# Optimization experiments

Measured on AMD Instinct MI355X. Metric: run time of the kernel, lower is better.

## Reference

```python
import jax, jax.numpy as jnp
import numpy as np

NEG_SLOPE = 0.2


def _gcn_conv(x, edge_index, W, b):
    # Standard GCNConv: y = D^-1/2 (A + I) D^-1/2 (x W) + b
    N = x.shape[0]
    loop = jnp.arange(N, dtype=edge_index.dtype)
    src = jnp.concatenate([edge_index[0], loop])  # [E+N]
    dst = jnp.concatenate([edge_index[1], loop])  # [E+N]
    deg = jax.ops.segment_sum(jnp.ones_like(dst, dtype=x.dtype), dst, num_segments=N)
    dinv = jnp.where(deg > 0, jax.lax.rsqrt(deg), 0.0)
    norm = dinv[src] * dinv[dst]                  # [E+N]
    h = x @ W                                     # [N, out] dense GEMM
    msg = h[src] * norm[:, None]                  # irregular gather, [E+N, out]
    agg = jax.ops.segment_sum(msg, dst, num_segments=N)  # irregular scatter
    return agg + b


def setup_inputs() -> dict:
    key = jax.random.key(0)
    ks = jax.random.split(key, 5)
    N, E, d_in, d_hid = 50000, 800000, 256, 512
    s = lambda fan_in, fan_out: np.sqrt(6.0 / (fan_in + fan_out))
    return {
        "x": jax.random.normal(ks[0], (N, d_in), dtype=jnp.float32),
        "edge_index": jax.random.randint(ks[1], (2, E), 0, N, dtype=jnp.int64),
        "W_gcn": jax.random.uniform(ks[2], (d_in, d_hid), jnp.float32, -s(d_in, d_hid), s(d_in, d_hid)),
        "b_gcn": jnp.zeros((d_hid,), jnp.float32),
        "W2": jax.random.uniform(ks[3], (d_hid, d_hid), jnp.float32, -s(d_hid, d_hid), s(d_hid, d_hid)),
        "b2": jnp.zeros((d_hid,), jnp.float32),
        "W_out": jax.random.uniform(ks[4], (d_hid, 1), jnp.float32, -s(d_hid, 1), s(d_hid, 1)),
        "b_out": jnp.zeros((1,), jnp.float32),
    }


def reference(x, edge_index, W_gcn, b_gcn, W2, b2, W_out, b_out):
    h = _gcn_conv(x, edge_index, W_gcn, b_gcn)           # [N, 512]
    h = jax.nn.leaky_relu(h, NEG_SLOPE)
    h = jax.nn.leaky_relu(h @ W2 + b2, NEG_SLOPE)        # [N, 512]
    return h @ W_out + b_out                             # [N, 1]
```

## Files before the change

kernel.cpp:

```cpp
#include <hip/hip_runtime.h>

#define D_IN  256
#define D_HID 512
#define NEG_SLOPE 0.2f
#define CAP 64
#define OVF_MAX 65536

typedef __attribute__((ext_vector_type(8))) short short8;
typedef __attribute__((ext_vector_type(4))) float floatx4;

__device__ __forceinline__ unsigned short f2bf(float f) {
    unsigned int u = __float_as_uint(f);
    u += 0x7fffu + ((u >> 16) & 1u);
    return (unsigned short)(u >> 16);
}
__device__ __forceinline__ float bf2f(unsigned short u) {
    return __uint_as_float(((unsigned int)u) << 16);
}

__device__ __forceinline__ int eidx(const void* ei, long pos, int is64) {
    return is64 ? (int)((const long long*)ei)[pos] : ((const int*)ei)[pos];
}

__global__ __launch_bounds__(256) void k_init(const float* __restrict__ x,
                                              unsigned short* __restrict__ xb,
                                              int* __restrict__ deg, int N,
                                              const unsigned int* __restrict__ ei,
                                              int npairs, int* flag, int* ovfcnt,
                                              const float* __restrict__ b_out,
                                              float* __restrict__ out,
                                              const float* __restrict__ Wa,
                                              unsigned short* __restrict__ Wat,
                                              const float* __restrict__ Wb,
                                              unsigned short* __restrict__ Wbt,
                                              long xthreads) {
    __shared__ float tl[64][65];
    int b = blockIdx.x;
    if (b < 96) {
        const float* W; unsigned short* Wt; int K, Nc, tk, tn;
        if (b < 32) { W = Wa; Wt = Wat; K = 256; Nc = 512; tk = b & 3; tn = b >> 2; }
        else { b -= 32; W = Wb; Wt = Wbt; K = 512; Nc = 512; tk = b & 7; tn = b >> 3; }
        int k0 = tk * 64, n0 = tn * 64;
        int c = threadIdx.x & 63;
        int r0 = threadIdx.x >> 6;
#pragma unroll
        for (int i = 0; i < 16; ++i) {
            int r = r0 + i * 4;
            tl[r][c] = W[(long)(k0 + r) * Nc + n0 + c];
        }
        __syncthreads();
#pragma unroll
        for (int i = 0; i < 16; ++i) {
            int r = r0 + i * 4;
            Wt[(long)(n0 + r) * K + k0 + c] = f2bf(tl[c][r]);
        }
        return;
    }
    if (b == 96) {
        __shared__ int nz;
        if (threadIdx.x == 0) nz = 0;
        __syncthreads();
        for (int p = threadIdx.x; p < npairs; p += blockDim.x)
            if (ei[2 * p + 1] != 0) nz = 1;
        __syncthreads();
        if (threadIdx.x == 0) { *flag = nz ? 0 : 1; *ovfcnt = 0; }
    }
    long t = (long)(b - 96) * 256 + threadIdx.x;
    if (t < xthreads) {
        long i = t * 4;
        float4 v = *(const float4*)(x + i);
        ushort4 o;
        o.x = f2bf(v.x); o.y = f2bf(v.y); o.z = f2bf(v.z); o.w = f2bf(v.w);
        *(ushort4*)(xb + i) = o;
    }
    if (t < N) { deg[t] = 0; out[t] = b_out[0]; }
}

__global__ void k_degfill(const void* __restrict__ ei, const int* __restrict__ flag,
                          int* __restrict__ deg, int* __restrict__ esrc,
                          int2* __restrict__ ovf, int* __restrict__ ovfcnt, int E) {
    int e = blockIdx.x * blockDim.x + threadIdx.x;
    if (e >= E) return;
    int is64 = *flag;
    int s = eidx(ei, e, is64), d = eidx(ei, (long)E + e, is64);
    int r = atomicAdd(&deg[d], 1);
    if (r < CAP) {
        esrc[d * CAP + r] = s;
    } else {
        int p = atomicAdd(ovfcnt, 1);
        if (p < OVF_MAX) ovf[p] = make_int2(d, s);
    }
}

__global__ __launch_bounds__(256) void k_dinv(const int* __restrict__ deg,
                                              float* __restrict__ dinv, int N) {
    int i = blockIdx.x * blockDim.x + threadIdx.x;
    if (i < N) dinv[i] = rsqrtf(1.0f + (float)deg[i]);
}

__global__ __launch_bounds__(256) void k_gather(const unsigned short* __restrict__ xb,
                                                const int* __restrict__ deg,
                                                const int* __restrict__ esrc,
                                                const float* __restrict__ dinv,
                                                const int2* __restrict__ ovf,
                                                const int* __restrict__ ovfcnt,
                                                unsigned short* __restrict__ aggb, int N) {
    int node = blockIdx.x * 4 + (threadIdx.x >> 6);
    int lane = threadIdx.x & 63;
    if (node >= N) return;
    int half = lane >> 5;
    int li   = lane & 31;
    int colofs = li * 8;
    float di = dinv[node];

    float a[8];
    {
        short8 v = *(const short8*)(xb + (long)node * D_IN + colofs);
#pragma unroll
        for (int j = 0; j < 8; ++j)
            a[j] = (half == 0) ? di * bf2f((unsigned short)v[j]) : 0.f;
    }

    int cnt = deg[node];
    if (cnt > CAP) cnt = CAP;
    int beg = node * CAP, end = beg + cnt;
    int e = beg;
    for (; e + 8 <= end; e += 8) {
        int s0 = esrc[e + half];
        int s1 = esrc[e + 2 + half];
        int s2 = esrc[e + 4 + half];
        int s3 = esrc[e + 6 + half];
        float w0 = dinv[s0], w1 = dinv[s1], w2 = dinv[s2], w3 = dinv[s3];
        short8 u0 = *(const short8*)(xb + (long)s0 * D_IN + colofs);
        short8 u1 = *(const short8*)(xb + (long)s1 * D_IN + colofs);
        short8 u2 = *(const short8*)(xb + (long)s2 * D_IN + colofs);
        short8 u3 = *(const short8*)(xb + (long)s3 * D_IN + colofs);
#pragma unroll
        for (int j = 0; j < 8; ++j)
            a[j] += w0 * bf2f((unsigned short)u0[j]) + w1 * bf2f((unsigned short)u1[j])
                  + w2 * bf2f((unsigned short)u2[j]) + w3 * bf2f((unsigned short)u3[j]);
    }
    for (; e < end; e += 2) {
        int j0 = e + half;
        int jj = (j0 < end) ? j0 : end - 1;
        int s = esrc[jj];
        float w = (j0 < end) ? dinv[s] : 0.f;
        short8 u = *(const short8*)(xb + (long)s * D_IN + colofs);
#pragma unroll
        for (int j = 0; j < 8; ++j)
            a[j] += w * bf2f((unsigned short)u[j]);
    }

    int oc = *ovfcnt;
    if (oc > OVF_MAX) oc = OVF_MAX;
    for (int i = 0; i < oc; ++i) {
        int2 p = ovf[i];
        if (p.x == node && half == 0) {
            float w = dinv[p.y];
            short8 u = *(const short8*)(xb + (long)p.y * D_IN + colofs);
#pragma unroll
            for (int j = 0; j < 8; ++j)
                a[j] += w * bf2f((unsigned short)u[j]);
        }
    }

#pragma unroll
    for (int j = 0; j < 8; ++j) a[j] += __shfl_xor(a[j], 32, 64);

    if (half == 0) {
        short8 o;
#pragma unroll
        for (int j = 0; j < 8; ++j) o[j] = (short)f2bf(a[j] * di);
        *(short8*)(aggb + (long)node * D_IN + colofs) = o;
    }
}

__device__ __forceinline__ void async_cp16(const unsigned short* gp, unsigned short* lp) {
    __builtin_amdgcn_global_load_lds((const __attribute__((address_space(1))) void*)gp,
                                     (__attribute__((address_space(3))) void*)lp, 16, 0, 0);
}

__device__ __forceinline__ void stage_sw64(const unsigned short* src, int strideK,
                                           int rowMax, unsigned short* lds, int tid) {
#pragma unroll
    for (int rr = 0; rr < 4; ++rr) {
        int c = rr * 256 + tid;
        int row = c >> 3;
        int ci = (c & 7) ^ (row & 7);
        if (row > rowMax) row = rowMax;
        async_cp16(src + (long)row * strideK + ci * 8, lds + c * 8);
    }
}

__device__ __forceinline__ bool map_block(int b, int M, int& m0, int& n0) {
    int x = b & 7, slot = b >> 3;
    int mt = x + 8 * (slot >> 2);
    m0 = mt * 128; n0 = (slot & 3) * 128;
    return m0 < M;
}

__device__ __forceinline__ void mfma_step(const unsigned short* As_,
                                          const unsigned short* Bs_,
                                          floatx4 acc[4][4],
                                          int wm, int wn, int r, int q, int xv) {
#pragma unroll
    for (int s = 0; s < 2; ++s) {
        int slotbase = s * 4 + q;
        short8 af[4], bf[4];
#pragma unroll
        for (int i = 0; i < 4; ++i)
            af[i] = *(const short8*)(As_ + (wm + i * 16 + r) * 64 + (slotbase ^ xv) * 8);
#pragma unroll
        for (int j = 0; j < 4; ++j)
            bf[j] = *(const short8*)(Bs_ + (wn + j * 16 + r) * 64 + (slotbase ^ xv) * 8);
#pragma unroll
        for (int i = 0; i < 4; ++i)
#pragma unroll
            for (int j = 0; j < 4; ++j)
                acc[i][j] = __builtin_amdgcn_mfma_f32_16x16x32_bf16(af[i], bf[j], acc[i][j], 0, 0, 0);
    }
}

#define GEMM_KLOOP(Ab, Bb, K, rmA)                                              \
    const int nt = (K) >> 6;                                                    \
    stage_sw64((Ab), (K), (rmA), As[0], tid);                                   \
    stage_sw64((Bb), (K), 127, Bs[0], tid);                                     \
    if (nt > 1) {                                                               \
        stage_sw64((Ab) + 64, (K), (rmA), As[1], tid);                          \
        stage_sw64((Bb) + 64, (K), 127, Bs[1], tid);                            \
    }                                                                           \
    for (int t = 0; t < nt; ++t) {                                              \
        const int cur = t & 1;                                                  \
        if (t + 1 < nt) asm volatile("s_waitcnt vmcnt(8)" ::: "memory");        \
        else            asm volatile("s_waitcnt vmcnt(0)" ::: "memory");        \
        __builtin_amdgcn_sched_barrier(0);                                      \
        __builtin_amdgcn_s_barrier();                                           \
        __builtin_amdgcn_sched_barrier(0);                                      \
        mfma_step(As[cur], Bs[cur], acc, wm, wn, r, q, xv);                     \
        __builtin_amdgcn_sched_barrier(0);                                      \
        __builtin_amdgcn_s_barrier();                                           \
        __builtin_amdgcn_sched_barrier(0);                                      \
        if (t + 2 < nt) {                                                       \
            stage_sw64((Ab) + (long)(t + 2) * 64, (K), (rmA), As[cur], tid);    \
            stage_sw64((Bb) + (long)(t + 2) * 64, (K), 127, Bs[cur], tid);      \
        }                                                                       \
    }

__global__ __launch_bounds__(256) void k_gemm_bf16(const unsigned short* __restrict__ A,
                                                   const unsigned short* __restrict__ Bt,
                                                   const float* __restrict__ bias,
                                                   unsigned short* __restrict__ C,
                                                   int M, int K) {
    __shared__ __align__(16) unsigned short As[2][128 * 64];
    __shared__ __align__(16) unsigned short Bs[2][128 * 64];
    __shared__ __align__(16) unsigned short Ep[32 * 128];
    const int tid  = threadIdx.x;
    const int lane = tid & 63, wave = tid >> 6;
    int m0, n0;
    if (!map_block(blockIdx.x, M, m0, n0)) return;
    const int r = lane & 15, q = lane >> 4;
    const int xv = r & 7;
    const int wm = (wave & 1) * 64, wn = (wave >> 1) * 64;
    const int band = wm >> 6;
    const int rmA = M - 1 - m0;
    const unsigned short* Ab = A + (long)m0 * K;
    const unsigned short* Bb = Bt + (long)n0 * K;

    floatx4 acc[4][4];
#pragma unroll
    for (int i = 0; i < 4; ++i)
#pragma unroll
        for (int j = 0; j < 4; ++j) acc[i][j] = (floatx4){0.f, 0.f, 0.f, 0.f};

    GEMM_KLOOP(Ab, Bb, K, rmA)

    float bv[4];
#pragma unroll
    for (int j = 0; j < 4; ++j) bv[j] = bias[n0 + wn + j * 16 + r];

#pragma unroll
    for (int i = 0; i < 4; ++i) {
#pragma unroll
        for (int j = 0; j < 4; ++j) {
#pragma unroll
            for (int t2 = 0; t2 < 4; ++t2) {
                float v = acc[i][j][t2] + bv[j];
                v = v > 0.f ? v : NEG_SLOPE * v;
                Ep[(band * 16 + q * 4 + t2) * 128 + wn + j * 16 + r] = f2bf(v);
            }
        }
        __syncthreads();
#pragma unroll
        for (int rr = 0; rr < 2; ++rr) {
            int c = rr * 256 + tid;
            int lrow = c >> 4, ccol = c & 15;
            int grow = m0 + (lrow >> 4) * 64 + i * 16 + (lrow & 15);
            if (grow < M) {
                short8 v = *(const short8*)(Ep + lrow * 128 + ccol * 8);
                *(short8*)(C + (long)grow * D_HID + n0 + ccol * 8) = v;
            }
        }
        __syncthreads();
    }
}

__global__ __launch_bounds__(256) void k_gemm2f(const unsigned short* __restrict__ A,
                                                const unsigned short* __restrict__ Bt,
                                                const float* __restrict__ bias,
                                                const float* __restrict__ wout,
                                                float* __restrict__ out,
                                                int M, int K) {
    __shared__ __align__(16) unsigned short As[2][128 * 64];
    __shared__ __align__(16) unsigned short Bs[2][128 * 64];
    const int tid  = threadIdx.x;
    const int lane = tid & 63, wave = tid >> 6;
    int m0, n0;
    if (!map_block(blockIdx.x, M, m0, n0)) return;
    const int r = lane & 15, q = lane >> 4;
    const int xv = r & 7;
    const int wm = (wave & 1) * 64, wn = (wave >> 1) * 64;
    const int rmA = M - 1 - m0;
    const unsigned short* Ab = A + (long)m0 * K;
    const unsigned short* Bb = Bt + (long)n0 * K;

    floatx4 acc[4][4];
#pragma unroll
    for (int i = 0; i < 4; ++i)
#pragma unroll
        for (int j = 0; j < 4; ++j) acc[i][j] = (floatx4){0.f, 0.f, 0.f, 0.f};

    GEMM_KLOOP(Ab, Bb, K, rmA)

    float bv[4], wv[4];
#pragma unroll
    for (int j = 0; j < 4; ++j) {
        int col = n0 + wn + j * 16 + r;
        bv[j] = bias[col];
        wv[j] = wout[col];
    }
#pragma unroll
    for (int i = 0; i < 4; ++i) {
#pragma unroll
        for (int t2 = 0; t2 < 4; ++t2) {
            float p = 0.f;
#pragma unroll
            for (int j = 0; j < 4; ++j) {
                float v = acc[i][j][t2] + bv[j];
                v = v > 0.f ? v : NEG_SLOPE * v;
                p += v * wv[j];
            }
            p += __shfl_xor(p, 8, 64);
            p += __shfl_xor(p, 4, 64);
            p += __shfl_xor(p, 2, 64);
            p += __shfl_xor(p, 1, 64);
            if (r == 0) {
                int row = m0 + wm + i * 16 + q * 4 + t2;
                if (row < M) atomicAdd(&out[row], p);
            }
        }
    }
}

extern "C" void kernel_launch(void* const* d_in, const int* in_sizes, int n_in,
                              void* d_out, int out_size, void* d_ws, size_t ws_size,
                              hipStream_t stream) {
    const float* x     = (const float*)d_in[0];
    const void*  ei    = d_in[1];
    const float* W_gcn = (const float*)d_in[2];
    const float* b_gcn = (const float*)d_in[3];
    const float* W2    = (const float*)d_in[4];
    const float* b2    = (const float*)d_in[5];
    const float* W_out = (const float*)d_in[6];
    const float* b_out = (const float*)d_in[7];
    float* out = (float*)d_out;

    const int N = in_sizes[0] / D_IN;
    const int E = in_sizes[1] / 2;

    char* w = (char*)d_ws;
    size_t off = 0;
    auto alloc = [&](size_t bytes) { char* p = w + off; off = (off + bytes + 255) & ~(size_t)255; return p; };
    int*            flag   = (int*)alloc(256);
    int*            ovfcnt = (int*)alloc(256);
    float*          dinv   = (float*)alloc((size_t)N * 4);
    int*            deg_i  = (int*)alloc((size_t)N * 4);
    int2*           ovf    = (int2*)alloc((size_t)OVF_MAX * 8);
    int*            esrc   = (int*)alloc((size_t)N * CAP * 4);
    unsigned short* xb     = (unsigned short*)alloc((size_t)N * D_IN * 2);
    unsigned short* aggb   = (unsigned short*)alloc((size_t)N * D_IN * 2);
    unsigned short* h1     = (unsigned short*)alloc((size_t)N * D_HID * 2);
    unsigned short* Wgt    = (unsigned short*)alloc((size_t)D_IN * D_HID * 2);
    unsigned short* W2t    = (unsigned short*)alloc((size_t)D_HID * D_HID * 2);

    int npairs = E < 2048 ? E : 2048;
    long xthreads = (long)N * D_IN / 4;
    int init_blocks = 96 + (int)((xthreads + 255) / 256);
    k_init<<<init_blocks, 256, 0, stream>>>(x, xb, deg_i, N, (const unsigned int*)ei,
                                            npairs, flag, ovfcnt, b_out, out,
                                            W_gcn, Wgt, W2, W2t, xthreads);

    k_degfill<<<(E + 255) / 256, 256, 0, stream>>>(ei, flag, deg_i, esrc, ovf, ovfcnt, E);
    k_dinv<<<(N + 255) / 256, 256, 0, stream>>>(deg_i, dinv, N);

    k_gather<<<(N + 3) / 4, 256, 0, stream>>>(xb, deg_i, esrc, dinv, ovf, ovfcnt, aggb, N);

    int mtiles = (N + 127) / 128;
    int gblocks = ((mtiles + 7) / 8) * 8 * 4;
    k_gemm_bf16<<<gblocks, 256, 0, stream>>>(aggb, Wgt, b_gcn, h1, N, D_IN);
    k_gemm2f<<<gblocks, 256, 0, stream>>>(h1, W2t, b2, W_out, out, N, D_HID);
}
```

Before: 281.2 us.

## Loop over all N-tiles per GEMM block and compute dinv inline

Each GEMM block now owns a full 128-row M-tile and loops over the four 128-column N-tiles itself, instead of one block per (M,N) tile. This lets the final GEMM reduce the output projection in shared memory and write out[] directly, dropping the atomics and the out initialization in k_init. The k_dinv kernel is removed; the gather recomputes rsqrt(1+deg) from deg on the fly. The launch grid shrinks by four times (about 391 blocks), which risks underfilling the GPU, and the A tile is re-streamed for every N-tile.

```diff
diff --git a/kernel.cpp b/kernel.cpp
--- a/kernel.cpp
+++ b/kernel.cpp
@@ -27,8 +27,6 @@
                                               int* __restrict__ deg, int N,
                                               const unsigned int* __restrict__ ei,
                                               int npairs, int* flag, int* ovfcnt,
-                                              const float* __restrict__ b_out,
-                                              float* __restrict__ out,
                                               const float* __restrict__ Wa,
                                               unsigned short* __restrict__ Wat,
                                               const float* __restrict__ Wb,
@@ -73,7 +71,7 @@
         o.x = f2bf(v.x); o.y = f2bf(v.y); o.z = f2bf(v.z); o.w = f2bf(v.w);
         *(ushort4*)(xb + i) = o;
     }
-    if (t < N) { deg[t] = 0; out[t] = b_out[0]; }
+    if (t < N) deg[t] = 0;
 }
 
 __global__ void k_degfill(const void* __restrict__ ei, const int* __restrict__ flag,
@@ -92,16 +90,9 @@
     }
 }
 
-__global__ __launch_bounds__(256) void k_dinv(const int* __restrict__ deg,
-                                              float* __restrict__ dinv, int N) {
-    int i = blockIdx.x * blockDim.x + threadIdx.x;
-    if (i < N) dinv[i] = rsqrtf(1.0f + (float)deg[i]);
-}
-
 __global__ __launch_bounds__(256) void k_gather(const unsigned short* __restrict__ xb,
                                                 const int* __restrict__ deg,
                                                 const int* __restrict__ esrc,
-                                                const float* __restrict__ dinv,
                                                 const int2* __restrict__ ovf,
                                                 const int* __restrict__ ovfcnt,
                                                 unsigned short* __restrict__ aggb, int N) {
@@ -111,7 +102,8 @@
     int half = lane >> 5;
     int li   = lane & 31;
     int colofs = li * 8;
-    float di = dinv[node];
+    int dn = deg[node];
+    float di = rsqrtf(1.0f + (float)dn);
 
     float a[8];
     {
@@ -121,8 +113,7 @@
             a[j] = (half == 0) ? di * bf2f((unsigned short)v[j]) : 0.f;
     }
 
-    int cnt = deg[node];
-    if (cnt > CAP) cnt = CAP;
+    int cnt = dn > CAP ? CAP : dn;
     int beg = node * CAP, end = beg + cnt;
     int e = beg;
     for (; e + 8 <= end; e += 8) {
@@ -130,7 +121,10 @@
         int s1 = esrc[e + 2 + half];
         int s2 = esrc[e + 4 + half];
         int s3 = esrc[e + 6 + half];
-        float w0 = dinv[s0], w1 = dinv[s1], w2 = dinv[s2], w3 = dinv[s3];
+        float w0 = rsqrtf(1.0f + (float)deg[s0]);
+        float w1 = rsqrtf(1.0f + (float)deg[s1]);
+        float w2 = rsqrtf(1.0f + (float)deg[s2]);
+        float w3 = rsqrtf(1.0f + (float)deg[s3]);
         short8 u0 = *(const short8*)(xb + (long)s0 * D_IN + colofs);
         short8 u1 = *(const short8*)(xb + (long)s1 * D_IN + colofs);
         short8 u2 = *(const short8*)(xb + (long)s2 * D_IN + colofs);
@@ -144,7 +138,7 @@
         int j0 = e + half;
         int jj = (j0 < end) ? j0 : end - 1;
         int s = esrc[jj];
-        float w = (j0 < end) ? dinv[s] : 0.f;
+        float w = (j0 < end) ? rsqrtf(1.0f + (float)deg[s]) : 0.f;
         short8 u = *(const short8*)(xb + (long)s * D_IN + colofs);
 #pragma unroll
         for (int j = 0; j < 8; ++j)
@@ -156,7 +150,7 @@
     for (int i = 0; i < oc; ++i) {
         int2 p = ovf[i];
         if (p.x == node && half == 0) {
-            float w = dinv[p.y];
+            float w = rsqrtf(1.0f + (float)deg[p.y]);
             short8 u = *(const short8*)(xb + (long)p.y * D_IN + colofs);
 #pragma unroll
             for (int j = 0; j < 8; ++j)
@@ -190,13 +184,6 @@
         if (row > rowMax) row = rowMax;
         async_cp16(src + (long)row * strideK + ci * 8, lds + c * 8);
     }
-}
-
-__device__ __forceinline__ bool map_block(int b, int M, int& m0, int& n0) {
-    int x = b & 7, slot = b >> 3;
-    int mt = x + 8 * (slot >> 2);
-    m0 = mt * 128; n0 = (slot & 3) * 128;
-    return m0 < M;
 }
 
 __device__ __forceinline__ void mfma_step(const unsigned short* As_,
@@ -256,51 +243,54 @@
     __shared__ __align__(16) unsigned short Ep[32 * 128];
     const int tid  = threadIdx.x;
     const int lane = tid & 63, wave = tid >> 6;
-    int m0, n0;
-    if (!map_block(blockIdx.x, M, m0, n0)) return;
+    const int m0 = blockIdx.x * 128;
+    if (m0 >= M) return;
     const int r = lane & 15, q = lane >> 4;
     const int xv = r & 7;
     const int wm = (wave & 1) * 64, wn = (wave >> 1) * 64;
     const int band = wm >> 6;
     const int rmA = M - 1 - m0;
     const unsigned short* Ab = A + (long)m0 * K;
-    const unsigned short* Bb = Bt + (long)n0 * K;
-
-    floatx4 acc[4][4];
-#pragma unroll
-    for (int i = 0; i < 4; ++i)
-#pragma unroll
-        for (int j = 0; j < 4; ++j) acc[i][j] = (floatx4){0.f, 0.f, 0.f, 0.f};
-
-    GEMM_KLOOP(Ab, Bb, K, rmA)
-
-    float bv[4];
-#pragma unroll
-    for (int j = 0; j < 4; ++j) bv[j] = bias[n0 + wn + j * 16 + r];
-
-#pragma unroll
-    for (int i = 0; i < 4; ++i) {
-#pragma unroll
-        for (int j = 0; j < 4; ++j) {
-#pragma unroll
-            for (int t2 = 0; t2 < 4; ++t2) {
-                float v = acc[i][j][t2] + bv[j];
-                v = v > 0.f ? v : NEG_SLOPE * v;
-                Ep[(band * 16 + q * 4 + t2) * 128 + wn + j * 16 + r] = f2bf(v);
+
+    for (int n0 = 0; n0 < D_HID; n0 += 128) {
+        const unsigned short* Bb = Bt + (long)n0 * K;
+
+        floatx4 acc[4][4];
+#pragma unroll
+        for (int i = 0; i < 4; ++i)
+#pragma unroll
+            for (int j = 0; j < 4; ++j) acc[i][j] = (floatx4){0.f, 0.f, 0.f, 0.f};
+
+        GEMM_KLOOP(Ab, Bb, K, rmA)
+
+        float bv[4];
+#pragma unroll
+        for (int j = 0; j < 4; ++j) bv[j] = bias[n0 + wn + j * 16 + r];
+
+#pragma unroll
+        for (int i = 0; i < 4; ++i) {
+#pragma unroll
+            for (int j = 0; j < 4; ++j) {
+#pragma unroll
+                for (int t2 = 0; t2 < 4; ++t2) {
+                    float v = acc[i][j][t2] + bv[j];
+                    v = v > 0.f ? v : NEG_SLOPE * v;
+                    Ep[(band * 16 + q * 4 + t2) * 128 + wn + j * 16 + r] = f2bf(v);
+                }
             }
-        }
-        __syncthreads();
-#pragma unroll
-        for (int rr = 0; rr < 2; ++rr) {
-            int c = rr * 256 + tid;
-            int lrow = c >> 4, ccol = c & 15;
-            int grow = m0 + (lrow >> 4) * 64 + i * 16 + (lrow & 15);
-            if (grow < M) {
-                short8 v = *(const short8*)(Ep + lrow * 128 + ccol * 8);
-                *(short8*)(C + (long)grow * D_HID + n0 + ccol * 8) = v;
+            __syncthreads();
+#pragma unroll
+            for (int rr = 0; rr < 2; ++rr) {
+                int c = rr * 256 + tid;
+                int lrow = c >> 4, ccol = c & 15;
+                int grow = m0 + (lrow >> 4) * 64 + i * 16 + (lrow & 15);
+                if (grow < M) {
+                    short8 v = *(const short8*)(Ep + lrow * 128 + ccol * 8);
+                    *(short8*)(C + (long)grow * D_HID + n0 + ccol * 8) = v;
+                }
             }
-        }
-        __syncthreads();
+            __syncthreads();
+        }
     }
 }
 
@@ -308,56 +298,79 @@
                                                 const unsigned short* __restrict__ Bt,
                                                 const float* __restrict__ bias,
                                                 const float* __restrict__ wout,
+                                                const float* __restrict__ b_out,
                                                 float* __restrict__ out,
                                                 int M, int K) {
     __shared__ __align__(16) unsigned short As[2][128 * 64];
     __shared__ __align__(16) unsigned short Bs[2][128 * 64];
+    __shared__ float pl[2][128];
     const int tid  = threadIdx.x;
     const int lane = tid & 63, wave = tid >> 6;
-    int m0, n0;
-    if (!map_block(blockIdx.x, M, m0, n0)) return;
+    const int m0 = blockIdx.x * 128;
+    if (m0 >= M) return;
     const int r = lane & 15, q = lane >> 4;
     const int xv = r & 7;
     const int wm = (wave & 1) * 64, wn = (wave >> 1) * 64;
     const int rmA = M - 1 - m0;
     const unsigned short* Ab = A + (long)m0 * K;
-    const unsigned short* Bb = Bt + (long)n0 * K;
-
-    floatx4 acc[4][4];
+
+    float preg[4][4];
 #pragma unroll
     for (int i = 0; i < 4; ++i)
 #pragma unroll
-        for (int j = 0; j < 4; ++j) acc[i][j] = (floatx4){0.f, 0.f, 0.f, 0.f};
-
-    GEMM_KLOOP(Ab, Bb, K, rmA)
-
-    float bv[4], wv[4];
-#pragma unroll
-    for (int j = 0; j < 4; ++j) {
-        int col = n0 + wn + j * 16 + r;
-        bv[j] = bias[col];
-        wv[j] = wout[col];
-    }
+        for (int t2 = 0; t2 < 4; ++t2) preg[i][t2] = 0.f;
+
+    for (int n0 = 0; n0 < D_HID; n0 += 128) {
+        const unsigned short* Bb = Bt + (long)n0 * K;
+
+        floatx4 acc[4][4];
+#pragma unroll
+        for (int i = 0; i < 4; ++i)
+#pragma unroll
+            for (int j = 0; j < 4; ++j) acc[i][j] = (floatx4){0.f, 0.f, 0.f, 0.f};
+
+        GEMM_KLOOP(Ab, Bb, K, rmA)
+
+        float bv[4], wv[4];
+#pragma unroll
+        for (int j = 0; j < 4; ++j) {
+            int col = n0 + wn + j * 16 + r;
+            bv[j] = bias[col];
+            wv[j] = wout[col];
+        }
+#pragma unroll
+        for (int i = 0; i < 4; ++i) {
+#pragma unroll
+            for (int t2 = 0; t2 < 4; ++t2) {
+                float p = 0.f;
+#pragma unroll
+                for (int j = 0; j < 4; ++j) {
+                    float v = acc[i][j][t2] + bv[j];
+                    v = v > 0.f ? v : NEG_SLOPE * v;
+                    p += v * wv[j];
+                }
+                preg[i][t2] += p;
+            }
+        }
+        __syncthreads();
+    }
+
 #pragma unroll
     for (int i = 0; i < 4; ++i) {
 #pragma unroll
         for (int t2 = 0; t2 < 4; ++t2) {
-            float p = 0.f;
-#pragma unroll
-            for (int j = 0; j < 4; ++j) {
-                float v = acc[i][j][t2] + bv[j];
-                v = v > 0.f ? v : NEG_SLOPE * v;
-                p += v * wv[j];
-            }
+            float p = preg[i][t2];
             p += __shfl_xor(p, 8, 64);
             p += __shfl_xor(p, 4, 64);
             p += __shfl_xor(p, 2, 64);
             p += __shfl_xor(p, 1, 64);
-            if (r == 0) {
-                int row = m0 + wm + i * 16 + q * 4 + t2;
-                if (row < M) atomicAdd(&out[row], p);
-            }
-        }
+            if (r == 0) pl[wn >> 6][wm + i * 16 + q * 4 + t2] = p;
+        }
+    }
+    __syncthreads();
+    if (tid < 128) {
+        int row = m0 + tid;
+        if (row < M) out[row] = b_out[0] + pl[0][tid] + pl[1][tid];
     }
 }
 
@@ -382,7 +395,6 @@
     auto alloc = [&](size_t bytes) { char* p = w + off; off = (off + bytes + 255) & ~(size_t)255; return p; };
     int*            flag   = (int*)alloc(256);
     int*            ovfcnt = (int*)alloc(256);
-    float*          dinv   = (float*)alloc((size_t)N * 4);
     int*            deg_i  = (int*)alloc((size_t)N * 4);
     int2*           ovf    = (int2*)alloc((size_t)OVF_MAX * 8);
     int*            esrc   = (int*)alloc((size_t)N * CAP * 4);
@@ -396,16 +408,14 @@
     long xthreads = (long)N * D_IN / 4;
     int init_blocks = 96 + (int)((xthreads + 255) / 256);
     k_init<<<init_blocks, 256, 0, stream>>>(x, xb, deg_i, N, (const unsigned int*)ei,
-                                            npairs, flag, ovfcnt, b_out, out,
+                                            npairs, flag, ovfcnt,
                                             W_gcn, Wgt, W2, W2t, xthreads);
 
     k_degfill<<<(E + 255) / 256, 256, 0, stream>>>(ei, flag, deg_i, esrc, ovf, ovfcnt, E);
-    k_dinv<<<(N + 255) / 256, 256, 0, stream>>>(deg_i, dinv, N);
-
-    k_gather<<<(N + 3) / 4, 256, 0, stream>>>(xb, deg_i, esrc, dinv, ovf, ovfcnt, aggb, N);
+
+    k_gather<<<(N + 3) / 4, 256, 0, stream>>>(xb, deg_i, esrc, ovf, ovfcnt, aggb, N);
 
     int mtiles = (N + 127) / 128;
-    int gblocks = ((mtiles + 7) / 8) * 8 * 4;
-    k_gemm_bf16<<<gblocks, 256, 0, stream>>>(aggb, Wgt, b_gcn, h1, N, D_IN);
-    k_gemm2f<<<gblocks, 256, 0, stream>>>(h1, W2t, b2, W_out, out, N, D_HID);
-}
+    k_gemm_bf16<<<mtiles, 256, 0, stream>>>(aggb, Wgt, b_gcn, h1, N, D_IN);
+    k_gemm2f<<<mtiles, 256, 0, stream>>>(h1, W2t, b2, W_out, b_out, out, N, D_HID);
+}
```

Measured after the change: 291.0 us. 3.5% more time.
